# Performance work log

Hardware: AMD Instinct MI355X
Metric: run time of the kernel (lower is better)

Reference implementation:

```python
import jax, jax.numpy as jnp
import numpy as np

B, S, H, A = 32, 2048, 1024, 256
NEG = jnp.float32(-1e20)


def setup_inputs() -> dict:
    key = jax.random.key(0)
    k = jax.random.split(key, 6)
    h_i = jax.random.normal(k[0], (B, S, H), jnp.float32)
    h_t = jax.random.normal(k[1], (B, H), jnp.float32)
    mask = jax.random.randint(k[2], (B, S), 0, 2).astype(bool)
    W = jax.random.normal(k[3], (A, 2 * H), jnp.float32) * 0.02
    b = jax.random.normal(k[4], (A,), jnp.float32) * 0.02
    u = jax.random.normal(k[5], (A, 1), jnp.float32)
    return {"h_i": h_i, "h_t": h_t, "mask": mask, "W": W, "b": b, "u": u}


def reference(h_i, h_t, mask, W, b, u):
    Bn, Sn, Hn = h_i.shape
    # h_t expanded along seq and concatenated: [B,S,2H]
    h_t_e = jnp.broadcast_to(h_t[:, None, :], (Bn, Sn, Hn))
    comb = jnp.concatenate([h_i, h_t_e], axis=-1)
    m = jnp.tanh(jnp.einsum('bsk,ak->bsa', comb, W) + b)  # [B,S,A]
    y = jnp.einsum('bsa,a->bs', m, u[:, 0])                # raw scores [B,S]
    # Faithful replication of torch masked_scatter per time step over the batch
    # dim: at step s, the masked batch positions receive SUCCESSIVE elements of
    # the score column y[:, s] (not necessarily the positionally aligned ones).
    pos = jnp.clip(jnp.cumsum(mask.astype(jnp.int32), axis=0) - 1, 0)  # [B,S]
    y_scattered = jnp.take_along_axis(y, pos, axis=0)
    beta = jnp.where(mask, y_scattered, NEG)
    alpha = jax.nn.softmax(beta, axis=1)                   # softmax over seq
    s = jnp.einsum('bs,bsh->bh', alpha, h_i)               # weighted sum [B,H]
    return s
```

## Files before the change

kernel.cpp:

```cpp
#include <hip/hip_runtime.h>
#include <math.h>

#define BB 32
#define SS 2048
#define HH 1024
#define AA 256
#define NEGV (-1e20f)
#define BK 32
#define CH 64
#define SCH (SS / CH)
#define NT (HH / BK)

typedef _Float16 half8 __attribute__((ext_vector_type(8)));
typedef float f32x4 __attribute__((ext_vector_type(4)));

__device__ inline void async_lds16(const void* g, void* l) {
    __builtin_amdgcn_global_load_lds(
        (const __attribute__((address_space(1))) unsigned int*)g,
        (__attribute__((address_space(3))) unsigned int*)l, 16, 0, 0);
}

__device__ inline half8 cvt8(float4 a, float4 b) {
    half8 h;
    h[0] = (_Float16)a.x; h[1] = (_Float16)a.y;
    h[2] = (_Float16)a.z; h[3] = (_Float16)a.w;
    h[4] = (_Float16)b.x; h[5] = (_Float16)b.y;
    h[6] = (_Float16)b.z; h[7] = (_Float16)b.w;
    return h;
}

__global__ __launch_bounds__(256) void k_prep(const float* __restrict__ W,
                                              const float* __restrict__ h_t,
                                              const float* __restrict__ bias,
                                              const int* __restrict__ mask,
                                              _Float16* __restrict__ W16t,
                                              float* __restrict__ c,
                                              int* __restrict__ sList,
                                              int* __restrict__ cntb,
                                              int* __restrict__ pcnt) {
    const int blk = blockIdx.x;
    const int tid = threadIdx.x;
    __shared__ int lcnt;

    if (blk < 128) {
        int idx = blk * 256 + tid;
        int kt = idx >> 10;
        int u  = idx & 1023;
        int col = u >> 2, ks = u & 3;
        const float* src = W + (size_t)col * 2 * HH + kt * BK + ks * 8;
        float4 a0 = *(const float4*)src;
        float4 a1 = *(const float4*)(src + 4);
        *reinterpret_cast<half8*>(W16t + (size_t)idx * 8) = cvt8(a0, a1);
        return;
    }
    if (blk < 2176) {
        int wave = tid >> 6;
        int lane = tid & 63;
        int pair = (blk - 128) * 4 + wave;
        int b = pair >> 8;
        int a = pair & (AA - 1);
        const float* ht = h_t + (size_t)b * HH;
        const float* w2 = W + (size_t)a * 2 * HH + HH;
        float acc = 0.f;
        for (int k = lane; k < HH; k += 64)
            acc += ht[k] * w2[k];
        for (int off = 32; off; off >>= 1)
            acc += __shfl_down(acc, off, 64);
        if (lane == 0) c[pair] = acc + bias[a];
        return;
    }
    const int b = blk - 2176;
    if (tid == 0) lcnt = 0;
    __syncthreads();
    int* lst = sList + b * SS;
#pragma unroll
    for (int i = 0; i < 8; ++i) {
        int s = tid + i * 256;
        int pref = 0, tot = 0;
#pragma unroll
        for (int bb = 0; bb < BB; ++bb) {
            int mv = (mask[bb * SS + s] != 0);
            tot += mv;
            if (bb <= b) pref += mv;
        }
        pcnt[b * SS + s] = pref;
        if (tot > b) { int p = atomicAdd(&lcnt, 1); lst[p] = s; }
    }
    __syncthreads();
    const int m = lcnt;
    if (tid == 0) cntb[b] = m;
    if (m > 0) {
        int padded = (m + 63) & ~63;
        int first = lst[0];
        for (int j = m + tid; j < padded; j += 256) lst[j] = first;
    }
}

__global__ __launch_bounds__(256, 2) void k2_mfma(const float* __restrict__ h_i,
                                                  const _Float16* __restrict__ W16t,
                                                  const float* __restrict__ c,
                                                  const float* __restrict__ u,
                                                  const int* __restrict__ sList,
                                                  const int* __restrict__ cntb,
                                                  float* __restrict__ y) {
    __shared__ _Float16 Alds[2][4][64][8];
    __shared__ _Float16 Blds[2][1024][8];
    __shared__ float c_s[AA], u_s[AA];
    __shared__ float red[2][64];
    __shared__ int s_idx[64];

    const int t = blockIdx.x;
    int b = -1, ti = 0, base = 0;
    for (int bb = 0; bb < BB; ++bb) {
        int nt = (cntb[bb] + 63) >> 6;
        if (b < 0 && t < base + nt) { b = bb; ti = t - base; }
        base += nt;
    }
    if (b < 0) return;

    const int tid = threadIdx.x;
    const int lane = tid & 63;
    const int wave = tid >> 6;
    const int wr = wave >> 1;
    const int wc = wave & 1;

    if (tid < 64) s_idx[tid] = sList[b * SS + ti * 64 + tid];
    c_s[tid] = c[b * AA + tid];
    u_s[tid] = u[tid];
    __syncthreads();

    f32x4 acc[2][8];
#pragma unroll
    for (int rf = 0; rf < 2; ++rf)
#pragma unroll
        for (int cf = 0; cf < 8; ++cf) acc[rf][cf] = (f32x4){0.f, 0.f, 0.f, 0.f};

    const int arow = tid >> 2;
    const int aks = tid & 3;
    const float* Abase = h_i + ((size_t)b * SS + s_idx[arow]) * HH + aks * 8;

    const int sb0 = __builtin_amdgcn_readfirstlane(wave * 256);
    _Float16* Bflat = &Blds[0][0][0];

    const int kq = lane >> 4;
    const int lr = lane & 15;

    {
#pragma unroll
        for (int i = 0; i < 4; ++i) {
            int sbase = sb0 + i * 64;
            async_lds16(W16t + (size_t)(sbase + lane) * 8,
                        Bflat + (size_t)sbase * 8);
        }
        float4 v0 = *(const float4*)Abase;
        float4 v1 = *(const float4*)(Abase + 4);
        *reinterpret_cast<half8*>(&Alds[0][aks][arow][0]) = cvt8(v0, v1);
    }
    __syncthreads();

    for (int t2 = 0; t2 < NT; ++t2) {
        const int cur = t2 & 1, nxt = cur ^ 1;
        const int k1 = (t2 + 1) * BK;
        float4 v0, v1;
        if (t2 < NT - 1) {
#pragma unroll
            for (int i = 0; i < 4; ++i) {
                int sbase = sb0 + i * 64;
                async_lds16(W16t + (size_t)(t2 + 1) * 8192 + (size_t)(sbase + lane) * 8,
                            Bflat + (size_t)nxt * 8192 + (size_t)sbase * 8);
            }
            v0 = *(const float4*)(Abase + k1);
            v1 = *(const float4*)(Abase + k1 + 4);
        }

        half8 af[2], bf[8];
#pragma unroll
        for (int rf = 0; rf < 2; ++rf)
            af[rf] = *reinterpret_cast<half8*>(&Alds[cur][kq][wr * 32 + rf * 16 + lr][0]);
#pragma unroll
        for (int cf = 0; cf < 8; ++cf) {
            int col = wc * 128 + cf * 16 + lr;
            bf[cf] = *reinterpret_cast<half8*>(
                Bflat + (size_t)cur * 8192 + (size_t)(col * 4 + kq) * 8);
        }
#pragma unroll
        for (int rf = 0; rf < 2; ++rf)
#pragma unroll
            for (int cf = 0; cf < 8; ++cf)
                acc[rf][cf] = __builtin_amdgcn_mfma_f32_16x16x32_f16(
                    af[rf], bf[cf], acc[rf][cf], 0, 0, 0);

        if (t2 < NT - 1) {
            *reinterpret_cast<half8*>(&Alds[nxt][aks][arow][0]) = cvt8(v0, v1);
        }
        __syncthreads();
    }

#pragma unroll
    for (int rf = 0; rf < 2; ++rf) {
#pragma unroll
        for (int j = 0; j < 4; ++j) {
            float v = 0.f;
#pragma unroll
            for (int cf = 0; cf < 8; ++cf) {
                int col = wc * 128 + cf * 16 + lr;
                float z = acc[rf][cf][j] + c_s[col];
                v += tanhf(z) * u_s[col];
            }
            v += __shfl_xor(v, 1, 64);
            v += __shfl_xor(v, 2, 64);
            v += __shfl_xor(v, 4, 64);
            v += __shfl_xor(v, 8, 64);
            if (lr == 0) red[wc][wr * 32 + rf * 16 + kq * 4 + j] = v;
        }
    }
    __syncthreads();
    if (tid < 64) y[(size_t)b * SS + s_idx[tid]] = red[0][tid] + red[1][tid];
}

__global__ __launch_bounds__(256) void k34(const float* __restrict__ h_i,
                                           const float* __restrict__ y,
                                           const int* __restrict__ mask,
                                           const int* __restrict__ pcnt,
                                           float* __restrict__ partial) {
    const int blk = blockIdx.x;
    const int b = blk >> 4;
    const int grp = blk & 15;
    const int tid = threadIdx.x;
    const int lane = tid & 63;
    const int wave = tid >> 6;
    __shared__ float rmax[4], rsum[4];
    __shared__ float aval[SCH];
    __shared__ int slist[SCH];
    __shared__ int mcnt;

    float beta[8];
    float mx = -INFINITY;
#pragma unroll
    for (int i = 0; i < 8; ++i) {
        int s = tid + i * 256;
        int p = pcnt[b * SS + s] - 1; if (p < 0) p = 0;
        float v = (mask[b * SS + s] != 0) ? y[(size_t)p * SS + s] : NEGV;
        beta[i] = v;
        mx = fmaxf(mx, v);
    }
    for (int off = 32; off; off >>= 1) mx = fmaxf(mx, __shfl_xor(mx, off, 64));
    if (lane == 0) rmax[wave] = mx;
    __syncthreads();
    mx = fmaxf(fmaxf(rmax[0], rmax[1]), fmaxf(rmax[2], rmax[3]));
    float sum = 0.f;
#pragma unroll
    for (int i = 0; i < 8; ++i) sum += expf(beta[i] - mx);
    for (int off = 32; off; off >>= 1) sum += __shfl_xor(sum, off, 64);
    if (lane == 0) rsum[wave] = sum;
    __syncthreads();
    sum = rsum[0] + rsum[1] + rsum[2] + rsum[3];
    const float inv = 1.f / sum;

    for (int cc = 0; cc < 4; ++cc) {
        const int ch = grp * 4 + cc;
        float a = 0.f;
        bool nz = false;
        if (tid < SCH) {
            int s = ch * SCH + tid;
            if (mask[b * SS + s] != 0) {
                int p = pcnt[b * SS + s] - 1; if (p < 0) p = 0;
                a = expf(y[(size_t)p * SS + s] - mx) * inv;
                nz = (a != 0.f);
            }
        }
        unsigned long long mk = __ballot(nz);
        if (tid < SCH) {
            int off = __popcll(mk & ((1ull << tid) - 1));
            if (nz) { slist[off] = tid; aval[off] = a; }
            if (tid == 0) mcnt = __popcll(mk);
        }
        __syncthreads();
        const int m = mcnt;
        const float* basep = h_i + (size_t)b * SS * HH + (size_t)ch * SCH * HH;
        f32x4 acc4 = {0.f, 0.f, 0.f, 0.f};
        for (int i2 = 0; i2 < m; ++i2) {
            float av = aval[i2];
            float4 v = *reinterpret_cast<const float4*>(
                &basep[(size_t)slist[i2] * HH + tid * 4]);
            acc4[0] += av * v.x; acc4[1] += av * v.y;
            acc4[2] += av * v.z; acc4[3] += av * v.w;
        }
        *reinterpret_cast<f32x4*>(
            &partial[((size_t)(b * CH + ch)) * HH + tid * 4]) = acc4;
        __syncthreads();
    }
}

__global__ __launch_bounds__(256) void k4b_reduce(const float* __restrict__ partial,
                                                  float* __restrict__ out) {
    int i = blockIdx.x * 256 + threadIdx.x;
    int b = i >> 10, h = i & (HH - 1);
    float s = 0.f;
#pragma unroll
    for (int ch = 0; ch < CH; ++ch)
        s += partial[((size_t)(b * CH + ch)) * HH + h];
    out[i] = s;
}

extern "C" void kernel_launch(void* const* d_in, const int* in_sizes, int n_in,
                              void* d_out, int out_size, void* d_ws, size_t ws_size,
                              hipStream_t stream) {
    const float* h_i  = (const float*)d_in[0];
    const float* h_t  = (const float*)d_in[1];
    const int*   mask = (const int*)d_in[2];
    const float* W    = (const float*)d_in[3];
    const float* bias = (const float*)d_in[4];
    const float* u    = (const float*)d_in[5];
    float* out = (float*)d_out;

    float* c        = (float*)d_ws;
    float* y        = c + BB * AA;
    float* partial  = y + BB * SS;
    _Float16* W16t  = (_Float16*)(partial + BB * CH * HH);
    int* sList      = (int*)(W16t + AA * HH);
    int* cntb       = sList + BB * SS;
    int* pcnt       = cntb + BB;

    k_prep<<<2208, 256, 0, stream>>>(W, h_t, bias, mask, W16t, c, sList, cntb, pcnt);
    k2_mfma<<<1024, 256, 0, stream>>>(h_i, W16t, c, u, sList, cntb, y);
    k34<<<BB * 16, 256, 0, stream>>>(h_i, y, mask, pcnt, partial);
    k4b_reduce<<<(BB * HH) / 256, 256, 0, stream>>>(partial, out);
}
```

Before: 120.2 us.

## Deepen h_i prefetch to triple-buffered LDS with manual waitcnt scheduling

Restructures the main GEMM loop so the fp32 h_i rows are loaded two K-tiles ahead through inline-asm global loads, converted to fp16 and stored into a three-slot LDS ring. Explicit vmcnt/lgkmcnt waits and raw s_barrier calls replace __syncthreads, so the MFMA work can overlap longer global-load latency. It also raises the launch-bounds occupancy hint from 2 to 3 blocks per CU and replaces per-thread LDS atomics in the list build with a wave ballot/popcount compaction. The hand-counted vmcnt values are fragile because the async LDS loads share the same counter, and the higher occupancy target may force register spills.

Measured after the change: 112.3 us. 6.5% less time.

```diff
diff --git a/kernel.cpp b/kernel.cpp
--- a/kernel.cpp
+++ b/kernel.cpp
@@ -20,7 +20,22 @@
         (__attribute__((address_space(3))) unsigned int*)l, 16, 0, 0);
 }
 
-__device__ inline half8 cvt8(float4 a, float4 b) {
+__device__ inline f32x4 gload4(const float* p) {
+    f32x4 r;
+    asm volatile("global_load_dwordx4 %0, %1, off"
+                 : "=&v"(r) : "v"(p) : "memory");
+    return r;
+}
+
+__device__ inline half8 cvt8(f32x4 a, f32x4 b) {
+    half8 h;
+    h[0] = (_Float16)a[0]; h[1] = (_Float16)a[1];
+    h[2] = (_Float16)a[2]; h[3] = (_Float16)a[3];
+    h[4] = (_Float16)b[0]; h[5] = (_Float16)b[1];
+    h[6] = (_Float16)b[2]; h[7] = (_Float16)b[3];
+    return h;
+}
+__device__ inline half8 cvt8f(float4 a, float4 b) {
     half8 h;
     h[0] = (_Float16)a.x; h[1] = (_Float16)a.y;
     h[2] = (_Float16)a.z; h[3] = (_Float16)a.w;
@@ -50,7 +65,7 @@
         const float* src = W + (size_t)col * 2 * HH + kt * BK + ks * 8;
         float4 a0 = *(const float4*)src;
         float4 a1 = *(const float4*)(src + 4);
-        *reinterpret_cast<half8*>(W16t + (size_t)idx * 8) = cvt8(a0, a1);
+        *reinterpret_cast<half8*>(W16t + (size_t)idx * 8) = cvt8f(a0, a1);
         return;
     }
     if (blk < 2176) {
@@ -70,6 +85,7 @@
         return;
     }
     const int b = blk - 2176;
+    const int lane = tid & 63;
     if (tid == 0) lcnt = 0;
     __syncthreads();
     int* lst = sList + b * SS;
@@ -84,7 +100,12 @@
             if (bb <= b) pref += mv;
         }
         pcnt[b * SS + s] = pref;
-        if (tot > b) { int p = atomicAdd(&lcnt, 1); lst[p] = s; }
+        bool need = (tot > b);
+        unsigned long long mk = __ballot(need);
+        int wbase = 0;
+        if (lane == 0) wbase = atomicAdd(&lcnt, __popcll(mk));
+        wbase = __shfl(wbase, 0, 64);
+        if (need) lst[wbase + __popcll(mk & ((1ull << lane) - 1))] = s;
     }
     __syncthreads();
     const int m = lcnt;
@@ -96,14 +117,14 @@
     }
 }
 
-__global__ __launch_bounds__(256, 2) void k2_mfma(const float* __restrict__ h_i,
+__global__ __launch_bounds__(256, 3) void k2_mfma(const float* __restrict__ h_i,
                                                   const _Float16* __restrict__ W16t,
                                                   const float* __restrict__ c,
                                                   const float* __restrict__ u,
                                                   const int* __restrict__ sList,
                                                   const int* __restrict__ cntb,
                                                   float* __restrict__ y) {
-    __shared__ _Float16 Alds[2][4][64][8];
+    __shared__ _Float16 Alds[3][4][64][8];
     __shared__ _Float16 Blds[2][1024][8];
     __shared__ float c_s[AA], u_s[AA];
     __shared__ float red[2][64];
@@ -145,43 +166,54 @@
     const int kq = lane >> 4;
     const int lr = lane & 15;
 
-    {
-#pragma unroll
-        for (int i = 0; i < 4; ++i) {
-            int sbase = sb0 + i * 64;
-            async_lds16(W16t + (size_t)(sbase + lane) * 8,
-                        Bflat + (size_t)sbase * 8);
-        }
-        float4 v0 = *(const float4*)Abase;
-        float4 v1 = *(const float4*)(Abase + 4);
-        *reinterpret_cast<half8*>(&Alds[0][aks][arow][0]) = cvt8(v0, v1);
-    }
-    __syncthreads();
+    f32x4 r0a = gload4(Abase);
+    f32x4 r0b = gload4(Abase + 4);
+    f32x4 r1a = gload4(Abase + BK);
+    f32x4 r1b = gload4(Abase + BK + 4);
+#pragma unroll
+    for (int i = 0; i < 4; ++i) {
+        int sbase = sb0 + i * 64;
+        async_lds16(W16t + (size_t)(sbase + lane) * 8, Bflat + (size_t)sbase * 8);
+    }
+    f32x4 rAa = gload4(Abase + 2 * BK);
+    f32x4 rAb = gload4(Abase + 2 * BK + 4);
+
+    asm volatile("s_waitcnt vmcnt(6)" ::: "memory");
+    __builtin_amdgcn_sched_barrier(0);
+    *reinterpret_cast<half8*>(&Alds[0][aks][arow][0]) = cvt8(r0a, r0b);
+    *reinterpret_cast<half8*>(&Alds[1][aks][arow][0]) = cvt8(r1a, r1b);
+    asm volatile("s_waitcnt vmcnt(2) lgkmcnt(0)" ::: "memory");
+    __builtin_amdgcn_sched_barrier(0);
+    __builtin_amdgcn_s_barrier();
 
     for (int t2 = 0; t2 < NT; ++t2) {
-        const int cur = t2 & 1, nxt = cur ^ 1;
-        const int k1 = (t2 + 1) * BK;
-        float4 v0, v1;
-        if (t2 < NT - 1) {
+        const int cur3 = t2 % 3, curB = t2 & 1;
+        if (t2 + 1 < NT) {
 #pragma unroll
             for (int i = 0; i < 4; ++i) {
                 int sbase = sb0 + i * 64;
                 async_lds16(W16t + (size_t)(t2 + 1) * 8192 + (size_t)(sbase + lane) * 8,
-                            Bflat + (size_t)nxt * 8192 + (size_t)sbase * 8);
+                            Bflat + (size_t)((t2 + 1) & 1) * 8192 + (size_t)sbase * 8);
             }
-            v0 = *(const float4*)(Abase + k1);
-            v1 = *(const float4*)(Abase + k1 + 4);
-        }
-
+        }
+        if (t2 + 2 < NT) {
+            asm volatile("s_waitcnt vmcnt(4)" ::: "memory");
+            __builtin_amdgcn_sched_barrier(0);
+            *reinterpret_cast<half8*>(&Alds[(t2 + 2) % 3][aks][arow][0]) = cvt8(rAa, rAb);
+        }
+        if (t2 + 3 < NT) {
+            rAa = gload4(Abase + (t2 + 3) * BK);
+            rAb = gload4(Abase + (t2 + 3) * BK + 4);
+        }
         half8 af[2], bf[8];
 #pragma unroll
         for (int rf = 0; rf < 2; ++rf)
-            af[rf] = *reinterpret_cast<half8*>(&Alds[cur][kq][wr * 32 + rf * 16 + lr][0]);
+            af[rf] = *reinterpret_cast<half8*>(&Alds[cur3][kq][wr * 32 + rf * 16 + lr][0]);
 #pragma unroll
         for (int cf = 0; cf < 8; ++cf) {
             int col = wc * 128 + cf * 16 + lr;
             bf[cf] = *reinterpret_cast<half8*>(
-                Bflat + (size_t)cur * 8192 + (size_t)(col * 4 + kq) * 8);
+                Bflat + (size_t)curB * 8192 + (size_t)(col * 4 + kq) * 8);
         }
 #pragma unroll
         for (int rf = 0; rf < 2; ++rf)
@@ -189,11 +221,14 @@
             for (int cf = 0; cf < 8; ++cf)
                 acc[rf][cf] = __builtin_amdgcn_mfma_f32_16x16x32_f16(
                     af[rf], bf[cf], acc[rf][cf], 0, 0, 0);
-
         if (t2 < NT - 1) {
-            *reinterpret_cast<half8*>(&Alds[nxt][aks][arow][0]) = cvt8(v0, v1);
-        }
-        __syncthreads();
+            if (t2 + 3 < NT)
+                asm volatile("s_waitcnt vmcnt(2) lgkmcnt(0)" ::: "memory");
+            else
+                asm volatile("s_waitcnt vmcnt(0) lgkmcnt(0)" ::: "memory");
+            __builtin_amdgcn_sched_barrier(0);
+            __builtin_amdgcn_s_barrier();
+        }
     }
 
 #pragma unroll
```
